# Optimization experiments

Measured on AMD Instinct MI355X. Metric: run time of the kernel, lower is better.

The kernel has to match this reference:

```python
import jax, jax.numpy as jnp
import numpy as np

B, F, R, O = 32768, 64, 64, 64  # batch, in_features, rules, out_features


def setup_inputs() -> dict:
    key = jax.random.key(0)
    k1, k2, k3, k4, k5 = jax.random.split(key, 5)
    X = jax.random.normal(k1, (B, F), dtype=jnp.float32)
    tt = jax.random.normal(k2, (1, F, R), dtype=jnp.float32) * 0.01
    mean = jax.random.normal(k3, (1, F, R), dtype=jnp.float32)
    # std is a learned positive scale (set by _rule_initialization); keep it away from 0
    std = jax.random.uniform(k4, (1, F, R), dtype=jnp.float32, minval=0.5, maxval=1.5)
    W = jax.random.normal(k5, (O, R * (F + 1)), dtype=jnp.float32) * 0.02  # nn.Linear weight [out, in]
    return {"X": X, "tt": tt, "mean": mean, "std": std, "W": W}


def reference(X, tt, mean, std, W):
    t = jnp.tanh(tt)                                  # [1,F,R]
    z = (X[:, :, None] - mean) / std                  # [B,F,R]
    g = jnp.exp(-(z * z))                             # Gaussian membership [B,F,R]
    m = g * t + 0.5 * (1.0 - t)                       # affine blend toward 0.5
    fire = jnp.prod(m, axis=1)                        # product t-norm over features -> [B,R]
    w = fire / jnp.sum(fire, axis=1, keepdims=True)   # normalize over rules
    ones = jnp.ones((X.shape[0], 1), dtype=X.dtype)
    Xa = jnp.concatenate([X, ones], axis=1)           # [B,F+1]
    feat = (Xa[:, :, None] * w[:, None, :]).reshape(X.shape[0], -1)  # [B,(F+1)*R], row-major (f outer, r inner)
    return feat @ W.T                                 # [B,O]
```

## Files before the change

kernel.cpp:

```cpp
#include <hip/hip_runtime.h>
#include <hip/hip_bf16.h>

#define F 64
#define R 64
#define O 64

typedef short bf16x8 __attribute__((ext_vector_type(8)));
typedef float f32x4 __attribute__((ext_vector_type(4)));
typedef float f32x2 __attribute__((ext_vector_type(2)));

static __device__ __forceinline__ unsigned short f2bf(float f) {
    unsigned u = __builtin_bit_cast(unsigned, f);
    unsigned r = (u + 0x7fffu + ((u >> 16) & 1u)) >> 16;
    return (unsigned short)r;
}

__global__ __launch_bounds__(256) void fq_prep(
        const float* __restrict__ tt, const float* __restrict__ mean,
        const float* __restrict__ std_, const float* __restrict__ W,
        float* __restrict__ prm, unsigned short* __restrict__ Wpk)
{
    const int tg = blockIdx.x * 256 + threadIdx.x;
    if (tg < 65 * 512) {
        const int f    = tg >> 9;
        const int u8   = tg & 511;
        const int lane = u8 & 63;
        const int kk   = (u8 >> 6) & 1;
        const int nt   = u8 >> 7;
        const int o    = nt * 16 + (lane & 15);
        const int rb   = ((lane >> 4) << 3) + kk * 32;
        const float* src = W + o * 4160 + f * 64 + rb;
        unsigned short v[8];
#pragma unroll
        for (int j = 0; j < 8; ++j) v[j] = f2bf(src[j]);
        const int dst = ((nt * 65 + f) * 2 + kk) * 64 + lane;
        *(bf16x8*)(Wpk + (size_t)dst * 8) = *(bf16x8*)v;
    } else if (tg < 65 * 512 + 4096) {
        const int u = tg - 65 * 512;
        float sd = std_[u];
        float mn = mean[u];
        float th = tanhf(tt[u]);
        float s  = 1.2011224087864498f / sd;
        float4 p;
        p.x = s;
        p.y = mn * s;
        p.z = th;
        p.w = 0.5f * (1.0f - th);
        ((float4*)prm)[u] = p;
    }
}

__global__ __launch_bounds__(256, 8) void fq_fire(
        const float* __restrict__ X,
        const float4* __restrict__ prm,
        unsigned short* __restrict__ fireb,
        float* __restrict__ rinvg)
{
    const int t    = threadIdx.x;
    const int lane = t & 63;
    const int w    = __builtin_amdgcn_readfirstlane(t >> 6);
    const int row0 = (blockIdx.x * 4 + w) * 4;

    f32x2 fire2[2] = {(f32x2){1.f, 1.f}, (f32x2){1.f, 1.f}};
    const float* Xw = X + (size_t)row0 * 64;
    float4 p = prm[lane];
#pragma unroll 4
    for (int f = 0; f < F; ++f) {
        const int pf = (f + 1 < 64) ? f + 1 : 63;
        float4 pn = prm[pf * 64 + lane];
        f32x2 px = (f32x2){p.x, p.x};
        f32x2 py = (f32x2){-p.y, -p.y};
        f32x2 pt = (f32x2){p.z, p.z};
        f32x2 pc = (f32x2){p.w, p.w};
#pragma unroll
        for (int i = 0; i < 2; ++i) {
            f32x2 x;
            x.x = Xw[(2 * i) * 64 + f];
            x.y = Xw[(2 * i + 1) * 64 + f];
            f32x2 z  = __builtin_elementwise_fma(x, px, py);
            f32x2 nz = -(z * z);
            f32x2 g;
            g.x = __builtin_amdgcn_exp2f(nz.x);
            g.y = __builtin_amdgcn_exp2f(nz.y);
            f32x2 m = __builtin_elementwise_fma(g, pt, pc);
            fire2[i] = fire2[i] * m;
        }
        p = pn;
    }

#pragma unroll
    for (int i = 0; i < 2; ++i) {
        fireb[(size_t)(row0 + 2 * i) * 64 + lane]     = f2bf(fire2[i].x);
        fireb[(size_t)(row0 + 2 * i + 1) * 64 + lane] = f2bf(fire2[i].y);
    }
#pragma unroll
    for (int i = 0; i < 2; ++i) {
        float sx = fire2[i].x, sy = fire2[i].y;
#pragma unroll
        for (int d = 1; d < 64; d <<= 1) {
            sx += __shfl_xor(sx, d);
            sy += __shfl_xor(sy, d);
        }
        if (lane == 0) {
            rinvg[row0 + 2 * i]     = 1.0f / sx;
            rinvg[row0 + 2 * i + 1] = 1.0f / sy;
        }
    }
}

__global__ __launch_bounds__(1024, 4) void fq_gemm(
        const float* __restrict__ X,
        const unsigned short* __restrict__ fireb,
        const float* __restrict__ rinvg,
        const bf16x8* __restrict__ Wp,
        float* __restrict__ out)
{
    __shared__ __align__(16) float xt[64][132];

    const int t    = threadIdx.x;
    const int lane = t & 63;
    const int w    = __builtin_amdgcn_readfirstlane(t >> 6);
    const int nt   = w >> 2;
    const int g    = w & 3;
    const int b0   = blockIdx.x * 128;

    const int m_in = lane & 15;
    const int quad = lane >> 4;
    const int q8   = quad * 8;
    const f32x4 z4 = (f32x4){0.f, 0.f, 0.f, 0.f};

    const bf16x8* wpb = Wp + (size_t)(nt * 130) * 64 + lane;
    bf16x8 pe0 = wpb[0 * 64],  pe1 = wpb[1 * 64];
    bf16x8 po0 = wpb[2 * 64],  po1 = wpb[3 * 64];

    bf16x8 wfrag[2][2];
    f32x4 rv[2];
#pragma unroll
    for (int mm = 0; mm < 2; ++mm) {
        const int myrow = b0 + 32 * g + 16 * mm + m_in;
        wfrag[mm][0] = *(const bf16x8*)(fireb + (size_t)myrow * 64 + q8);
        wfrag[mm][1] = *(const bf16x8*)(fireb + (size_t)myrow * 64 + q8 + 32);
        rv[mm] = *(const f32x4*)(rinvg + b0 + 32 * g + 16 * mm + quad * 4);
    }

    {
        const int xrow = t >> 3;
        const int xf8  = (t & 7) * 8;
        float4 x0 = *(const float4*)(X + (size_t)(b0 + xrow) * 64 + xf8);
        float4 x1 = *(const float4*)(X + (size_t)(b0 + xrow) * 64 + xf8 + 4);
#pragma unroll
        for (int j = 0; j < 4; ++j) {
            xt[xf8 + j][xrow]     = x0[j];
            xt[xf8 + 4 + j][xrow] = x1[j];
        }
    }
    __syncthreads();

    f32x4 acc[2];
    acc[0] = z4; acc[1] = z4;

#pragma unroll 2
    for (int i = 0; i < 32; ++i) {
        const int fe = 2 * i, fo = 2 * i + 1;
        bf16x8 ce0 = pe0, ce1 = pe1, co0 = po0, co1 = po1;
        const int se = (fe + 2 <= 64) ? fe + 2 : 64;
        const int so = (fo + 2 <= 64) ? fo + 2 : 64;
        pe0 = wpb[(2 * se) * 64];  pe1 = wpb[(2 * se + 1) * 64];
        po0 = wpb[(2 * so) * 64];  po1 = wpb[(2 * so + 1) * 64];
#pragma unroll
        for (int mm = 0; mm < 2; ++mm) {
            f32x4 U = __builtin_amdgcn_mfma_f32_16x16x32_bf16(wfrag[mm][0], ce0, z4, 0, 0, 0);
            U = __builtin_amdgcn_mfma_f32_16x16x32_bf16(wfrag[mm][1], ce1, U, 0, 0, 0);
            f32x4 xv = *(const f32x4*)&xt[fe][32 * g + 16 * mm + quad * 4];
#pragma unroll
            for (int reg = 0; reg < 4; ++reg)
                acc[mm][reg] = __builtin_fmaf(xv[reg], U[reg], acc[mm][reg]);
        }
#pragma unroll
        for (int mm = 0; mm < 2; ++mm) {
            f32x4 U = __builtin_amdgcn_mfma_f32_16x16x32_bf16(wfrag[mm][0], co0, z4, 0, 0, 0);
            U = __builtin_amdgcn_mfma_f32_16x16x32_bf16(wfrag[mm][1], co1, U, 0, 0, 0);
            f32x4 xv = *(const f32x4*)&xt[fo][32 * g + 16 * mm + quad * 4];
#pragma unroll
            for (int reg = 0; reg < 4; ++reg)
                acc[mm][reg] = __builtin_fmaf(xv[reg], U[reg], acc[mm][reg]);
        }
    }

#pragma unroll
    for (int mm = 0; mm < 2; ++mm) {
        f32x4 U = __builtin_amdgcn_mfma_f32_16x16x32_bf16(wfrag[mm][0], pe0, z4, 0, 0, 0);
        U = __builtin_amdgcn_mfma_f32_16x16x32_bf16(wfrag[mm][1], pe1, U, 0, 0, 0);
#pragma unroll
        for (int reg = 0; reg < 4; ++reg)
            acc[mm][reg] += U[reg];
    }

#pragma unroll
    for (int mm = 0; mm < 2; ++mm)
#pragma unroll
        for (int reg = 0; reg < 4; ++reg) {
            const int row = b0 + 32 * g + 16 * mm + quad * 4 + reg;
            out[(size_t)row * 64 + nt * 16 + m_in] = acc[mm][reg] * rv[mm][reg];
        }
}

extern "C" void kernel_launch(void* const* d_in, const int* in_sizes, int n_in,
                              void* d_out, int out_size, void* d_ws, size_t ws_size,
                              hipStream_t stream) {
    const float* X    = (const float*)d_in[0];
    const float* tt   = (const float*)d_in[1];
    const float* mean = (const float*)d_in[2];
    const float* std_ = (const float*)d_in[3];
    const float* W    = (const float*)d_in[4];
    float* out = (float*)d_out;

    float* prm           = (float*)d_ws;
    unsigned short* Wpk  = (unsigned short*)((char*)d_ws + 65536);
    unsigned short* fb   = (unsigned short*)((char*)d_ws + 655360);
    float* rinvg         = (float*)((char*)d_ws + 4849664);

    fq_prep<<<146, 256, 0, stream>>>(tt, mean, std_, W, prm, Wpk);
    fq_fire<<<2048, 256, 0, stream>>>(X, (const float4*)prm, fb, rinvg);
    fq_gemm<<<256, 1024, 0, stream>>>(X, fb, rinvg, (const bf16x8*)Wpk, out);
}
```

Before: 112.3 us.

## Retile GEMM to 64-row blocks with each wave covering four M tiles

Changes fq_gemm from 1024-thread blocks over 128 rows, with waves split into 4 N-tiles x 4 row groups, to 256-thread blocks over 64 rows where each wave owns one N-tile and all four 16-row M tiles. Each W fragment load is now reused across four M tiles instead of two, which cuts the per-wave weight traffic per row, and the grid doubles to 512 blocks. In exchange each wave holds more registers for accumulators and fire fragments, and the smaller blocks may change occupancy.

```diff
diff --git a/kernel.cpp b/kernel.cpp
--- a/kernel.cpp
+++ b/kernel.cpp
@@ -108,21 +108,20 @@
     }
 }
 
-__global__ __launch_bounds__(1024, 4) void fq_gemm(
+__global__ __launch_bounds__(256, 2) void fq_gemm(
         const float* __restrict__ X,
         const unsigned short* __restrict__ fireb,
         const float* __restrict__ rinvg,
         const bf16x8* __restrict__ Wp,
         float* __restrict__ out)
 {
-    __shared__ __align__(16) float xt[64][132];
+    __shared__ __align__(16) float xt[64][68];
 
     const int t    = threadIdx.x;
     const int lane = t & 63;
     const int w    = __builtin_amdgcn_readfirstlane(t >> 6);
-    const int nt   = w >> 2;
-    const int g    = w & 3;
-    const int b0   = blockIdx.x * 128;
+    const int nt   = w;
+    const int b0   = blockIdx.x * 64;
 
     const int m_in = lane & 15;
     const int quad = lane >> 4;
@@ -133,31 +132,31 @@
     bf16x8 pe0 = wpb[0 * 64],  pe1 = wpb[1 * 64];
     bf16x8 po0 = wpb[2 * 64],  po1 = wpb[3 * 64];
 
-    bf16x8 wfrag[2][2];
-    f32x4 rv[2];
-#pragma unroll
-    for (int mm = 0; mm < 2; ++mm) {
-        const int myrow = b0 + 32 * g + 16 * mm + m_in;
-        wfrag[mm][0] = *(const bf16x8*)(fireb + (size_t)myrow * 64 + q8);
-        wfrag[mm][1] = *(const bf16x8*)(fireb + (size_t)myrow * 64 + q8 + 32);
-        rv[mm] = *(const f32x4*)(rinvg + b0 + 32 * g + 16 * mm + quad * 4);
+    bf16x8 wfrag[4][2];
+#pragma unroll
+    for (int m = 0; m < 4; ++m) {
+        const int myrow = b0 + 16 * m + m_in;
+        wfrag[m][0] = *(const bf16x8*)(fireb + (size_t)myrow * 64 + q8);
+        wfrag[m][1] = *(const bf16x8*)(fireb + (size_t)myrow * 64 + q8 + 32);
     }
 
     {
-        const int xrow = t >> 3;
-        const int xf8  = (t & 7) * 8;
-        float4 x0 = *(const float4*)(X + (size_t)(b0 + xrow) * 64 + xf8);
-        float4 x1 = *(const float4*)(X + (size_t)(b0 + xrow) * 64 + xf8 + 4);
-#pragma unroll
-        for (int j = 0; j < 4; ++j) {
-            xt[xf8 + j][xrow]     = x0[j];
-            xt[xf8 + 4 + j][xrow] = x1[j];
+        const int xrow = t >> 2;
+        const int xf16 = (t & 3) * 16;
+#pragma unroll
+        for (int c = 0; c < 4; ++c) {
+            float4 xv = *(const float4*)(X + (size_t)(b0 + xrow) * 64 + xf16 + 4 * c);
+            xt[xf16 + 4 * c + 0][xrow] = xv.x;
+            xt[xf16 + 4 * c + 1][xrow] = xv.y;
+            xt[xf16 + 4 * c + 2][xrow] = xv.z;
+            xt[xf16 + 4 * c + 3][xrow] = xv.w;
         }
     }
     __syncthreads();
 
-    f32x4 acc[2];
-    acc[0] = z4; acc[1] = z4;
+    f32x4 acc[4];
+#pragma unroll
+    for (int m = 0; m < 4; ++m) acc[m] = z4;
 
 #pragma unroll 2
     for (int i = 0; i < 32; ++i) {
@@ -168,41 +167,43 @@
         pe0 = wpb[(2 * se) * 64];  pe1 = wpb[(2 * se + 1) * 64];
         po0 = wpb[(2 * so) * 64];  po1 = wpb[(2 * so + 1) * 64];
 #pragma unroll
-        for (int mm = 0; mm < 2; ++mm) {
-            f32x4 U = __builtin_amdgcn_mfma_f32_16x16x32_bf16(wfrag[mm][0], ce0, z4, 0, 0, 0);
-            U = __builtin_amdgcn_mfma_f32_16x16x32_bf16(wfrag[mm][1], ce1, U, 0, 0, 0);
-            f32x4 xv = *(const f32x4*)&xt[fe][32 * g + 16 * mm + quad * 4];
+        for (int m = 0; m < 4; ++m) {
+            f32x4 U = __builtin_amdgcn_mfma_f32_16x16x32_bf16(wfrag[m][0], ce0, z4, 0, 0, 0);
+            U = __builtin_amdgcn_mfma_f32_16x16x32_bf16(wfrag[m][1], ce1, U, 0, 0, 0);
+            f32x4 xv = *(const f32x4*)&xt[fe][16 * m + quad * 4];
 #pragma unroll
             for (int reg = 0; reg < 4; ++reg)
-                acc[mm][reg] = __builtin_fmaf(xv[reg], U[reg], acc[mm][reg]);
-        }
-#pragma unroll
-        for (int mm = 0; mm < 2; ++mm) {
-            f32x4 U = __builtin_amdgcn_mfma_f32_16x16x32_bf16(wfrag[mm][0], co0, z4, 0, 0, 0);
-            U = __builtin_amdgcn_mfma_f32_16x16x32_bf16(wfrag[mm][1], co1, U, 0, 0, 0);
-            f32x4 xv = *(const f32x4*)&xt[fo][32 * g + 16 * mm + quad * 4];
+                acc[m][reg] = __builtin_fmaf(xv[reg], U[reg], acc[m][reg]);
+        }
+#pragma unroll
+        for (int m = 0; m < 4; ++m) {
+            f32x4 U = __builtin_amdgcn_mfma_f32_16x16x32_bf16(wfrag[m][0], co0, z4, 0, 0, 0);
+            U = __builtin_amdgcn_mfma_f32_16x16x32_bf16(wfrag[m][1], co1, U, 0, 0, 0);
+            f32x4 xv = *(const f32x4*)&xt[fo][16 * m + quad * 4];
 #pragma unroll
             for (int reg = 0; reg < 4; ++reg)
-                acc[mm][reg] = __builtin_fmaf(xv[reg], U[reg], acc[mm][reg]);
-        }
-    }
-
-#pragma unroll
-    for (int mm = 0; mm < 2; ++mm) {
-        f32x4 U = __builtin_amdgcn_mfma_f32_16x16x32_bf16(wfrag[mm][0], pe0, z4, 0, 0, 0);
-        U = __builtin_amdgcn_mfma_f32_16x16x32_bf16(wfrag[mm][1], pe1, U, 0, 0, 0);
+                acc[m][reg] = __builtin_fmaf(xv[reg], U[reg], acc[m][reg]);
+        }
+    }
+
+#pragma unroll
+    for (int m = 0; m < 4; ++m) {
+        f32x4 U = __builtin_amdgcn_mfma_f32_16x16x32_bf16(wfrag[m][0], pe0, z4, 0, 0, 0);
+        U = __builtin_amdgcn_mfma_f32_16x16x32_bf16(wfrag[m][1], pe1, U, 0, 0, 0);
 #pragma unroll
         for (int reg = 0; reg < 4; ++reg)
-            acc[mm][reg] += U[reg];
-    }
-
-#pragma unroll
-    for (int mm = 0; mm < 2; ++mm)
+            acc[m][reg] += U[reg];
+    }
+
+#pragma unroll
+    for (int m = 0; m < 4; ++m) {
+        f32x4 rv = *(const f32x4*)(rinvg + b0 + 16 * m + quad * 4);
 #pragma unroll
         for (int reg = 0; reg < 4; ++reg) {
-            const int row = b0 + 32 * g + 16 * mm + quad * 4 + reg;
-            out[(size_t)row * 64 + nt * 16 + m_in] = acc[mm][reg] * rv[mm][reg];
-        }
+            const int row = b0 + 16 * m + quad * 4 + reg;
+            out[(size_t)row * 64 + nt * 16 + m_in] = acc[m][reg] * rv[reg];
+        }
+    }
 }
 
 extern "C" void kernel_launch(void* const* d_in, const int* in_sizes, int n_in,
@@ -222,5 +223,5 @@
 
     fq_prep<<<146, 256, 0, stream>>>(tt, mean, std_, W, prm, Wpk);
     fq_fire<<<2048, 256, 0, stream>>>(X, (const float4*)prm, fb, rinvg);
-    fq_gemm<<<256, 1024, 0, stream>>>(X, fb, rinvg, (const bf16x8*)Wpk, out);
-}
+    fq_gemm<<<512, 256, 0, stream>>>(X, fb, rinvg, (const bf16x8*)Wpk, out);
+}
```

Result: no change. 113.5 us (+1.1%).
